# Kernel optimization log

Measured on AMD Instinct MI355X. Metric: run time of the kernel, lower is better.

Reference implementation:

```python
import jax, jax.numpy as jnp
import numpy as np
import math

HIDDEN = 512
NUM_HEADS = 16
HEAD_DIM = HIDDEN // NUM_HEADS          # 32
SPOW_DIM = HEAD_DIM * (HEAD_DIM + 1) // 2  # 528
GAMMA = 0.9
B, S = 2, 1024

_TRIU_I, _TRIU_J = np.triu_indices(HEAD_DIM, k=1)
_SQRT2 = math.sqrt(2.0)


def spow2(x):
    # x: (..., d) -> (..., d*(d+1)//2); squares then sqrt(2)*upper-tri cross terms
    squares = x * x
    cross = _SQRT2 * (x[..., _TRIU_I] * x[..., _TRIU_J])
    return jnp.concatenate([squares, cross], axis=-1)


def setup_inputs() -> dict:
    key = jax.random.key(0)
    ks = jax.random.split(key, 9)
    lim = 1.0 / math.sqrt(HIDDEN)
    w = lambda k: jax.random.uniform(k, (HIDDEN, HIDDEN), jnp.float32, -lim, lim)
    b = lambda k: jax.random.uniform(k, (HIDDEN,), jnp.float32, -lim, lim)
    return {
        "x": jax.random.normal(ks[0], (B, S, HIDDEN), jnp.float32),
        "q_w": w(ks[1]), "q_b": b(ks[2]),
        "k_w": w(ks[3]), "k_b": b(ks[4]),
        "v_w": w(ks[5]), "v_b": b(ks[6]),
        "o_w": w(ks[7]), "o_b": b(ks[8]),
    }


def reference(x, q_w, q_b, k_w, k_b, v_w, v_b, o_w, o_b):
    Bb, Ss, Hh = x.shape
    q = (x @ q_w + q_b).reshape(Bb, Ss, NUM_HEADS, HEAD_DIM)
    k = (x @ k_w + k_b).reshape(Bb, Ss, NUM_HEADS, HEAD_DIM)
    v = (x @ v_w + v_b).reshape(Bb, Ss, NUM_HEADS, HEAD_DIM)

    sq = spow2(q)  # [B,S,H,Dspow]
    sk = spow2(k)  # [B,S,H,Dspow]

    # time-major for scan
    sq_t = jnp.moveaxis(sq, 1, 0)  # [S,B,H,D]
    sk_t = jnp.moveaxis(sk, 1, 0)
    v_t = jnp.moveaxis(v, 1, 0)    # [S,B,H,hd]

    state0 = jnp.zeros((Bb, NUM_HEADS, SPOW_DIM, HEAD_DIM), x.dtype)

    def step(state, inp):
        skt, sqt, vt = inp
        # state = gamma*state + spow_k \otimes v  -> [B,H,Dspow,hd]
        state = GAMMA * state + skt[..., :, None] * vt[..., None, :]
        out = jnp.einsum('bhD,bhDd->bhd', sqt, state)
        return state, out

    _, outs = jax.lax.scan(step, state0, (sk_t, sq_t, v_t))  # [S,B,H,hd]
    out = jnp.moveaxis(outs, 0, 1).reshape(Bb, Ss, Hh)
    return out @ o_w + o_b
```

## Files before the change

kernel.cpp:

```cpp
#include <hip/hip_runtime.h>
#include <hip/hip_bf16.h>
#include <math.h>

#define HIDDEN 512
#define NHEADS 16
#define HDIM   32
#define BATCH  2
#define SEQ    1024
#define MROWS  (BATCH * SEQ)

constexpr float LOG2_GAMMA = -0.15200309344504997f;

typedef __hip_bfloat16 bf16;
typedef __attribute__((ext_vector_type(8))) short short8;
typedef __attribute__((ext_vector_type(4))) float f32x4;

__device__ __forceinline__ void async16(const void* g, void* l) {
    __builtin_amdgcn_global_load_lds(
        (const __attribute__((address_space(1))) void*)g,
        (__attribute__((address_space(3))) void*)l, 16, 0, 0);
}

__device__ __forceinline__ unsigned short f2bf_bits(float f) {
    bf16 b = __float2bfloat16(f);
    return *(unsigned short*)&b;
}

__global__ __launch_bounds__(256) void prep(
    const float* __restrict__ x,
    const float* __restrict__ qw, const float* __restrict__ kw,
    const float* __restrict__ vw, const float* __restrict__ ow,
    bf16* __restrict__ xb, bf16* __restrict__ wqkvt, bf16* __restrict__ wot)
{
    const int blk = blockIdx.x, tid = threadIdx.x;
    if (blk < 256) {
        const int widx = blk >> 6;
        const int tile = blk & 63;
        const int tk = (tile & 7) * 64, tn = (tile >> 3) * 64;
        const float* w = widx == 0 ? qw : widx == 1 ? kw : widx == 2 ? vw : ow;
        __shared__ float t[64][65];
        #pragma unroll
        for (int u = 0; u < 4; ++u) {
            const int r = u * 16 + (tid >> 4);
            const int c = (tid & 15) * 4;
            float4 v = *(const float4*)&w[(size_t)(tk + r) * 512 + tn + c];
            t[r][c + 0] = v.x; t[r][c + 1] = v.y; t[r][c + 2] = v.z; t[r][c + 3] = v.w;
        }
        __syncthreads();
        #pragma unroll
        for (int u = 0; u < 2; ++u) {
            const int rr = u * 32 + (tid >> 3);
            const int cc = (tid & 7) * 8;
            alignas(16) unsigned short tmp[8];
            #pragma unroll
            for (int i = 0; i < 8; ++i) tmp[i] = f2bf_bits(t[cc + i][rr]);
            bf16* dst = (widx < 3)
                ? &wqkvt[((size_t)widx * 512 + tn + rr) * 512 + tk + cc]
                : &wot[(size_t)(tn + rr) * 512 + tk + cc];
            *(short8*)dst = *(short8*)tmp;
        }
    } else {
        #pragma unroll
        for (int u = 0; u < 4; ++u) {
            const int idx = (blk - 256) * 1024 + u * 256 + tid;
            float4 v = ((const float4*)x)[idx];
            unsigned pk0 = (unsigned)f2bf_bits(v.x) | ((unsigned)f2bf_bits(v.y) << 16);
            unsigned pk1 = (unsigned)f2bf_bits(v.z) | ((unsigned)f2bf_bits(v.w) << 16);
            uint2 pk = {pk0, pk1};
            *(uint2*)&xb[(size_t)idx * 4] = pk;
        }
    }
}

template<int MS, int EPI>
__global__ __launch_bounds__(256) void gemm_persistB(
    const bf16* __restrict__ A, const bf16* __restrict__ Bt,
    const float* __restrict__ b0, const float* __restrict__ b1,
    const float* __restrict__ b2,
    float* __restrict__ Cf, bf16* __restrict__ Cb, int ldc)
{
    constexpr int K = 512;
    constexpr int LDB = 520;
    constexpr int TM = MS / 64;
    __shared__ alignas(16) short Bs[64 * LDB];

    const int tid = threadIdx.x;
    const int wave = tid >> 6, lane = tid & 63;
    const int fr = lane & 15, quad = lane >> 4;
    const int n0 = blockIdx.x * 64;
    const int m0 = blockIdx.y * MS;

    #pragma unroll
    for (int i = 0; i < 16; ++i) {
        const int row = wave * 16 + i;
        async16(&Bt[(size_t)(n0 + row) * K + lane * 8], &Bs[row * LDB]);
    }
    __syncthreads();

    const bf16* pa = &A[(size_t)(m0 + wave * (MS / 4) + fr) * K + quad * 8];

    f32x4 acc[TM][4] = {};
    #pragma unroll
    for (int ks = 0; ks < 16; ++ks) {
        short8 bfrag[4];
        #pragma unroll
        for (int j = 0; j < 4; ++j)
            bfrag[j] = *(const short8*)&Bs[(j * 16 + fr) * LDB + ks * 32 + quad * 8];
        #pragma unroll
        for (int i = 0; i < TM; ++i) {
            short8 af = *(const short8*)(pa + (size_t)i * 16 * K + ks * 32);
            #pragma unroll
            for (int j = 0; j < 4; ++j)
                acc[i][j] = __builtin_amdgcn_mfma_f32_16x16x32_bf16(
                    af, bfrag[j], acc[i][j], 0, 0, 0);
        }
    }

    if (EPI == 1) {
        const int seg = n0 >> 9;
        const float* bp = seg == 0 ? b0 : seg == 1 ? b1 : b2;
        const float sgn = seg == 0 ? 0.5f : seg == 1 ? -0.5f : 0.0f;
        #pragma unroll
        for (int i = 0; i < TM; ++i) {
            const int mrow = m0 + wave * (MS / 4) + i * 16 + quad * 4;
            float sc[4];
            #pragma unroll
            for (int r = 0; r < 4; ++r)
                sc[r] = exp2f((float)((mrow + r) & 63) * (sgn * LOG2_GAMMA));
            #pragma unroll
            for (int j = 0; j < 4; ++j) {
                const int n = n0 + j * 16 + fr;
                const float bv = bp[n & 511];
                #pragma unroll
                for (int r = 0; r < 4; ++r) {
                    unsigned short h = f2bf_bits((acc[i][j][r] + bv) * sc[r]);
                    *(unsigned short*)&Cb[(size_t)(mrow + r) * ldc + n] = h;
                }
            }
        }
    } else {
        #pragma unroll
        for (int i = 0; i < TM; ++i) {
            const int mrow = m0 + wave * (MS / 4) + i * 16 + quad * 4;
            #pragma unroll
            for (int j = 0; j < 4; ++j) {
                const int n = n0 + j * 16 + fr;
                const float bv = b0[n];
                #pragma unroll
                for (int r = 0; r < 4; ++r)
                    Cf[(size_t)(mrow + r) * ldc + n] = acc[i][j][r] + bv;
            }
        }
    }
}

__global__ __launch_bounds__(256) void power_attn_mfma(
    const bf16* __restrict__ qkv, bf16* __restrict__ atc)
{
    __shared__ alignas(16) short Qs[64 * 32];
    __shared__ alignas(16) short Ks[64 * 32];
    __shared__ alignas(16) short Vt[32 * 80];
    __shared__ alignas(16) short Ps[64 * 72];

    const int tid = threadIdx.x, wave = tid >> 6, lane = tid & 63;
    const int chunk = blockIdx.x, bh = blockIdx.y;
    const int b = bh >> 4, h = bh & 15;
    const int mb = b * SEQ + chunk * 64;
    const int fr = lane & 15, quad = lane >> 4;

    async16(&qkv[(size_t)(mb + wave * 16 + (lane >> 2)) * 1536 + h * 32 + (lane & 3) * 8],
            &Qs[wave * 512]);

    f32x4 o0 = {}, o1 = {};
    const int jstart = chunk >= 2 ? chunk - 2 : 0;

    for (int j = jstart; j <= chunk; ++j) {
        __syncthreads();
        const int sb = b * SEQ + j * 64;
        async16(&qkv[(size_t)(sb + wave * 16 + (lane >> 2)) * 1536 + 512 + h * 32 + (lane & 3) * 8],
                &Ks[wave * 512]);
        if (tid < 128) {
            const int p = tid >> 2, s = p * 2, dbase = (tid & 3) * 8;
            const short* g = (const short*)&qkv[(size_t)(sb + s) * 1536 + 1024 + h * 32 + dbase];
            short8 v0 = *(const short8*)g;
            short8 v1 = *(const short8*)(g + 1536);
            #pragma unroll
            for (int i = 0; i < 8; ++i) {
                unsigned pk = (unsigned)(unsigned short)v0[i]
                            | ((unsigned)(unsigned short)v1[i] << 16);
                *(unsigned*)&Vt[(dbase + i) * 80 + s] = pk;
            }
        }
        __syncthreads();

        short8 aq = *(const short8*)&Qs[(wave * 16 + fr) * 32 + quad * 8];
        f32x4 sAcc[4] = {};
        #pragma unroll
        for (int nt = 0; nt < 4; ++nt) {
            short8 bk = *(const short8*)&Ks[(nt * 16 + fr) * 32 + quad * 8];
            sAcc[nt] = __builtin_amdgcn_mfma_f32_16x16x32_bf16(aq, bk, sAcc[nt], 0, 0, 0);
        }

        const int dj = chunk - j;
        const float sj = exp2f(64.0f * (float)dj * LOG2_GAMMA);
        const int tbase = wave * 16 + quad * 4;
        #pragma unroll
        for (int nt = 0; nt < 4; ++nt) {
            const int s_l = nt * 16 + fr;
            #pragma unroll
            for (int r = 0; r < 4; ++r) {
                const int t_l = tbase + r;
                float pv = sAcc[nt][r];
                pv = pv * pv * sj;
                if (dj == 0 && s_l > t_l) pv = 0.0f;
                Ps[t_l * 72 + s_l] = (short)f2bf_bits(pv);
            }
        }
        short8 a0 = *(const short8*)&Ps[(wave * 16 + fr) * 72 + quad * 8];
        short8 a1 = *(const short8*)&Ps[(wave * 16 + fr) * 72 + 32 + quad * 8];
        short8 b00 = *(const short8*)&Vt[fr * 80 + quad * 8];
        short8 b01 = *(const short8*)&Vt[fr * 80 + 32 + quad * 8];
        short8 b10 = *(const short8*)&Vt[(16 + fr) * 80 + quad * 8];
        short8 b11 = *(const short8*)&Vt[(16 + fr) * 80 + 32 + quad * 8];
        o0 = __builtin_amdgcn_mfma_f32_16x16x32_bf16(a0, b00, o0, 0, 0, 0);
        o0 = __builtin_amdgcn_mfma_f32_16x16x32_bf16(a1, b01, o0, 0, 0, 0);
        o1 = __builtin_amdgcn_mfma_f32_16x16x32_bf16(a0, b10, o1, 0, 0, 0);
        o1 = __builtin_amdgcn_mfma_f32_16x16x32_bf16(a1, b11, o1, 0, 0, 0);
    }

    #pragma unroll
    for (int r = 0; r < 4; ++r) {
        const size_t row = mb + wave * 16 + quad * 4 + r;
        const int col = h * 32 + fr;
        *(unsigned short*)&atc[row * 512 + col]      = f2bf_bits(o0[r]);
        *(unsigned short*)&atc[row * 512 + col + 16] = f2bf_bits(o1[r]);
    }
}

extern "C" void kernel_launch(void* const* d_in, const int* in_sizes, int n_in,
                              void* d_out, int out_size, void* d_ws, size_t ws_size,
                              hipStream_t stream)
{
    const float* x  = (const float*)d_in[0];
    const float* qw = (const float*)d_in[1];
    const float* qb = (const float*)d_in[2];
    const float* kw = (const float*)d_in[3];
    const float* kb = (const float*)d_in[4];
    const float* vw = (const float*)d_in[5];
    const float* vb = (const float*)d_in[6];
    const float* ow = (const float*)d_in[7];
    const float* ob = (const float*)d_in[8];
    float* out = (float*)d_out;

    char* w = (char*)d_ws;
    bf16* xb    = (bf16*)(w);
    bf16* wqkvt = (bf16*)(w + (2ull  << 20));
    bf16* wot   = (bf16*)(w + (2ull  << 20) + (1536ull << 10));
    bf16* qkvb  = (bf16*)(w + (4ull  << 20));
    bf16* atc   = (bf16*)(w + (10ull << 20));

    prep<<<512, 256, 0, stream>>>(x, qw, kw, vw, ow, xb, wqkvt, wot);

    gemm_persistB<128, 1><<<dim3(1536 / 64, MROWS / 128), 256, 0, stream>>>(
        xb, wqkvt, qb, kb, vb, nullptr, qkvb, 1536);

    power_attn_mfma<<<dim3(SEQ / 64, BATCH * NHEADS), 256, 0, stream>>>(qkvb, atc);

    gemm_persistB<64, 0><<<dim3(512 / 64, MROWS / 64), 256, 0, stream>>>(
        atc, wot, ob, nullptr, nullptr, out, nullptr, 512);
}
```

Before: 98.27 us.

## Fuse four kernels into one persistent kernel with global atomic barriers

Merges the prep, QKV GEMM, attention and output GEMM kernels into a single 512-block launch, with each stage separated by an atomic grid-wide barrier. Shared memory is one buffer sized for the largest stage and reused by every stage. The aim is to remove three kernel launch gaps and their ramp-up and drain tails. In exchange it relies on all 512 blocks being resident at once (two per CU under the launch bounds) to avoid deadlock, and it adds a memset launch plus spin-wait barrier cost.

```diff
diff --git a/kernel.cpp b/kernel.cpp
--- a/kernel.cpp
+++ b/kernel.cpp
@@ -8,6 +8,7 @@
 #define BATCH  2
 #define SEQ    1024
 #define MROWS  (BATCH * SEQ)
+#define NBLK   512
 
 constexpr float LOG2_GAMMA = -0.15200309344504997f;
 
@@ -26,19 +27,31 @@
     return *(unsigned short*)&b;
 }
 
-__global__ __launch_bounds__(256) void prep(
+__device__ __forceinline__ void gbar(int* bar, int phase, int tid) {
+    __syncthreads();
+    if (tid == 0) {
+        __hip_atomic_fetch_add(bar, 1, __ATOMIC_ACQ_REL, __HIP_MEMORY_SCOPE_AGENT);
+        while (__hip_atomic_load(bar, __ATOMIC_ACQUIRE, __HIP_MEMORY_SCOPE_AGENT)
+               < phase * NBLK) {
+            __builtin_amdgcn_s_sleep(8);
+        }
+    }
+    __syncthreads();
+}
+
+__device__ __forceinline__ void prep_body(
+    char* smem, int blk, int tid,
     const float* __restrict__ x,
     const float* __restrict__ qw, const float* __restrict__ kw,
     const float* __restrict__ vw, const float* __restrict__ ow,
     bf16* __restrict__ xb, bf16* __restrict__ wqkvt, bf16* __restrict__ wot)
 {
-    const int blk = blockIdx.x, tid = threadIdx.x;
     if (blk < 256) {
+        float (*t)[65] = (float(*)[65])smem;
         const int widx = blk >> 6;
         const int tile = blk & 63;
         const int tk = (tile & 7) * 64, tn = (tile >> 3) * 64;
         const float* w = widx == 0 ? qw : widx == 1 ? kw : widx == 2 ? vw : ow;
-        __shared__ float t[64][65];
         #pragma unroll
         for (int u = 0; u < 4; ++u) {
             const int r = u * 16 + (tid >> 4);
@@ -73,7 +86,8 @@
 }
 
 template<int MS, int EPI>
-__global__ __launch_bounds__(256) void gemm_persistB(
+__device__ __forceinline__ void gemm_body(
+    short* Bs, int bx, int by, int tid,
     const bf16* __restrict__ A, const bf16* __restrict__ Bt,
     const float* __restrict__ b0, const float* __restrict__ b1,
     const float* __restrict__ b2,
@@ -82,13 +96,11 @@
     constexpr int K = 512;
     constexpr int LDB = 520;
     constexpr int TM = MS / 64;
-    __shared__ alignas(16) short Bs[64 * LDB];
-
-    const int tid = threadIdx.x;
+
     const int wave = tid >> 6, lane = tid & 63;
     const int fr = lane & 15, quad = lane >> 4;
-    const int n0 = blockIdx.x * 64;
-    const int m0 = blockIdx.y * MS;
+    const int n0 = bx * 64;
+    const int m0 = by * MS;
 
     #pragma unroll
     for (int i = 0; i < 16; ++i) {
@@ -154,16 +166,16 @@
     }
 }
 
-__global__ __launch_bounds__(256) void power_attn_mfma(
+__device__ __forceinline__ void attn_body(
+    char* smem, int chunk, int bh, int tid,
     const bf16* __restrict__ qkv, bf16* __restrict__ atc)
 {
-    __shared__ alignas(16) short Qs[64 * 32];
-    __shared__ alignas(16) short Ks[64 * 32];
-    __shared__ alignas(16) short Vt[32 * 80];
-    __shared__ alignas(16) short Ps[64 * 72];
-
-    const int tid = threadIdx.x, wave = tid >> 6, lane = tid & 63;
-    const int chunk = blockIdx.x, bh = blockIdx.y;
+    short* Qs = (short*)smem;
+    short* Ks = (short*)(smem + 4096);
+    short* Vt = (short*)(smem + 8192);
+    short* Ps = (short*)(smem + 13312);
+
+    const int wave = tid >> 6, lane = tid & 63;
     const int b = bh >> 4, h = bh & 15;
     const int mb = b * SEQ + chunk * 64;
     const int fr = lane & 15, quad = lane >> 4;
@@ -237,6 +249,41 @@
     }
 }
 
+__global__ __launch_bounds__(256, 2) void fused_pipeline(
+    const float* __restrict__ x,
+    const float* __restrict__ qw, const float* __restrict__ kw,
+    const float* __restrict__ vw, const float* __restrict__ ow,
+    const float* __restrict__ qb, const float* __restrict__ kb,
+    const float* __restrict__ vb, const float* __restrict__ ob,
+    float* __restrict__ out,
+    bf16* __restrict__ xb, bf16* __restrict__ wqkvt, bf16* __restrict__ wot,
+    bf16* __restrict__ qkvb, bf16* __restrict__ atc,
+    int* __restrict__ bar)
+{
+    __shared__ alignas(16) char smem[64 * 520 * 2];
+
+    const int bid = blockIdx.x;
+    const int tid = threadIdx.x;
+
+    prep_body(smem, bid, tid, x, qw, kw, vw, ow, xb, wqkvt, wot);
+
+    gbar(bar, 1, tid);
+
+    if (bid < 384)
+        gemm_body<128, 1>((short*)smem, bid % 24, bid / 24, tid,
+                          xb, wqkvt, qb, kb, vb, nullptr, qkvb, 1536);
+
+    gbar(bar, 2, tid);
+
+    attn_body(smem, bid & 15, bid >> 4, tid, qkvb, atc);
+
+    gbar(bar, 3, tid);
+
+    if (bid < 256)
+        gemm_body<64, 0>((short*)smem, bid & 7, bid >> 3, tid,
+                         atc, wot, ob, nullptr, nullptr, out, nullptr, 512);
+}
+
 extern "C" void kernel_launch(void* const* d_in, const int* in_sizes, int n_in,
                               void* d_out, int out_size, void* d_ws, size_t ws_size,
                               hipStream_t stream)
@@ -258,14 +305,11 @@
     bf16* wot   = (bf16*)(w + (2ull  << 20) + (1536ull << 10));
     bf16* qkvb  = (bf16*)(w + (4ull  << 20));
     bf16* atc   = (bf16*)(w + (10ull << 20));
-
-    prep<<<512, 256, 0, stream>>>(x, qw, kw, vw, ow, xb, wqkvt, wot);
-
-    gemm_persistB<128, 1><<<dim3(1536 / 64, MROWS / 128), 256, 0, stream>>>(
-        xb, wqkvt, qb, kb, vb, nullptr, qkvb, 1536);
-
-    power_attn_mfma<<<dim3(SEQ / 64, BATCH * NHEADS), 256, 0, stream>>>(qkvb, atc);
-
-    gemm_persistB<64, 0><<<dim3(512 / 64, MROWS / 64), 256, 0, stream>>>(
-        atc, wot, ob, nullptr, nullptr, out, nullptr, 512);
-}
+    int*  bar   = (int*)(w + (12ull << 20));
+
+    hipMemsetAsync(bar, 0, 64, stream);
+
+    fused_pipeline<<<NBLK, 256, 0, stream>>>(
+        x, qw, kw, vw, ow, qb, kb, vb, ob, out,
+        xb, wqkvt, wot, qkvb, atc, bar);
+}
```

After: 264.6 us. 2.69x slower.
